# Optimization experiments

Hardware: AMD Instinct MI355X
Metric: run time of the kernel (lower is better)

## Reference

```python
import jax, jax.numpy as jnp
import numpy as np

B, T, D_MODEL = 4, 2048, 1024
D_EXPERT, N_EXPERTS, TOP_K = 4096, 8, 2
CAPACITY_FACTOR = 1.25
AUX_COEFF, Z_COEFF = 0.01, 0.001


def setup_inputs() -> dict:
    key = jax.random.key(0)
    k = jax.random.split(key, 4)
    x = jax.random.normal(k[0], (B, T, D_MODEL), jnp.float32)
    Wr = jax.random.normal(k[1], (D_MODEL, N_EXPERTS), jnp.float32) * 0.02
    W1 = jax.random.normal(k[2], (N_EXPERTS, D_MODEL, D_EXPERT), jnp.float32) * (1.0 / np.sqrt(D_MODEL))
    b1 = jnp.zeros((N_EXPERTS, D_EXPERT), jnp.float32)
    W2 = jax.random.normal(k[3], (N_EXPERTS, D_EXPERT, D_MODEL), jnp.float32) * (1.0 / np.sqrt(D_EXPERT))
    b2 = jnp.zeros((N_EXPERTS, D_MODEL), jnp.float32)
    return {"x": x, "Wr": Wr, "W1": W1, "b1": b1, "W2": W2, "b2": b2}


def reference(x, Wr, W1, b1, W2, b2):
    Bb, Tt, D = x.shape
    N = Bb * Tt
    E = W1.shape[0]
    capacity = max(1, int(N / E * CAPACITY_FACTOR * TOP_K))

    xf = x.reshape(N, D)
    logits = xf @ Wr                                    # (N, E)
    z_loss = jnp.mean(jax.nn.logsumexp(logits, axis=-1) ** 2)
    probs = jax.nn.softmax(logits, axis=-1)             # (N, E)

    topk_p, topk_i = jax.lax.top_k(probs, TOP_K)        # (N, K)
    # one-hot expert mask (top-k experts are distinct per token)
    mask = jnp.zeros((N, E), probs.dtype).at[jnp.arange(N)[:, None], topk_i].set(1.0)

    # capacity truncation: keep first `capacity` assigned tokens per expert, in token order
    pos = (jnp.cumsum(mask, axis=0) - mask).astype(jnp.int32)   # exclusive rank within expert
    keep = (pos < capacity) & (mask > 0)
    mask_t = jnp.where(keep, mask, jnp.zeros_like(mask))

    # Switch-style aux loss on truncated mask
    total_sel = jnp.maximum(mask_t.sum(), 1.0)
    f_i = mask_t.sum(axis=0) / total_sel
    P_i = probs.mean(axis=0)
    aux_loss = E * jnp.sum(f_i * P_i)

    # normalized top-k combine weights (differentiable through probs)
    tk_raw = jnp.take_along_axis(probs, topk_i, axis=1)          # (N, K)
    tk = tk_raw / jnp.maximum(tk_raw.sum(axis=-1, keepdims=True), 1e-9)

    # dispatch tokens into (E, capacity, D) buffer; dropped tokens scatter out of range
    pos_safe = jnp.where(keep, pos, capacity)                    # capacity -> dropped
    pos_k = jnp.take_along_axis(pos_safe, topk_i, axis=1)        # (N, K)
    upd = jnp.broadcast_to(xf[:, None, :], (N, TOP_K, D)).reshape(-1, D)
    buf = jnp.zeros((E, capacity, D), x.dtype).at[topk_i.reshape(-1), pos_k.reshape(-1)].set(upd, mode='drop')

    # grouped expert MLP
    h = jax.nn.relu(jnp.einsum('ecd,edf->ecf', buf, W1) + b1[:, None, :])
    eo = jnp.einsum('ecf,efd->ecd', h, W2) + b2[:, None, :]      # (E, capacity, D)

    # combine: gather each token's top-k expert outputs, weight, sum; dropped -> weight 0
    valid_k = jnp.take_along_axis(keep, topk_i, axis=1)          # (N, K) bool
    w = tk * valid_k.astype(tk.dtype)
    pos_g = jnp.minimum(pos_k, capacity - 1)
    gathered = eo[topk_i, pos_g]                                 # (N, K, D)
    out = jnp.einsum('nk,nkd->nd', w, gathered).reshape(Bb, Tt, D)

    total_aux = AUX_COEFF * aux_loss + Z_COEFF * z_loss
    return out, aux_loss, z_loss, total_aux
```

## Files before the change

kernel.cpp:

```cpp
#include <hip/hip_runtime.h>
#include <stdint.h>

#define N_TOK    8192
#define DM       1024
#define DE       4096
#define NEXP     8
#define CAP      2560
#define AUX_CO   0.01f
#define Z_CO     0.001f

typedef __attribute__((ext_vector_type(4))) float f32x4;
typedef __attribute__((ext_vector_type(8))) __bf16 bf16x8;

static __device__ __forceinline__ unsigned short f2bf(float f) {
  union { float f; uint32_t u; } v; v.f = f;
  uint32_t r = 0x7fffu + ((v.u >> 16) & 1u);
  return (unsigned short)((v.u + r) >> 16);
}
static __device__ __forceinline__ float bf2f(unsigned short u) {
  union { uint32_t u; float f; } v; v.u = ((uint32_t)u) << 16;
  return v.f;
}

#define MEMFENCE() asm volatile("" ::: "memory")
#define BAR()    do { MEMFENCE(); __builtin_amdgcn_s_barrier(); MEMFENCE(); } while (0)
#define LGKM0()  asm volatile("s_waitcnt lgkmcnt(0)" ::: "memory")
#define LGKM8()  asm volatile("s_waitcnt lgkmcnt(8)" ::: "memory")
#define VMW(N)   asm volatile("s_waitcnt vmcnt(" #N ")" ::: "memory")
#define SB0()    __builtin_amdgcn_sched_barrier(0)
#define GLD16(g, l) __builtin_amdgcn_global_load_lds( \
    (const __attribute__((address_space(1))) void*)(g), \
    (__attribute__((address_space(3))) void*)(l), 16, 0, 0)

__global__ __launch_bounds__(256) void transpose_to_bf16(
    const float* __restrict__ in, unsigned short* __restrict__ out, int R, int C)
{
  __shared__ float tile[64][65];
  const size_t eoff = (size_t)blockIdx.z * R * C;
  const int bx = blockIdx.x * 64, by = blockIdx.y * 64;
  const int r = threadIdx.x >> 2, c16 = (threadIdx.x & 3) * 16;
#pragma unroll
  for (int j = 0; j < 4; ++j) {
    const float4 v = *(const float4*)&in[eoff + (size_t)(by + r) * C + bx + c16 + j * 4];
    tile[r][c16 + j * 4 + 0] = v.x; tile[r][c16 + j * 4 + 1] = v.y;
    tile[r][c16 + j * 4 + 2] = v.z; tile[r][c16 + j * 4 + 3] = v.w;
  }
  __syncthreads();
  const int oc = threadIdx.x >> 2, r16 = (threadIdx.x & 3) * 16;
#pragma unroll
  for (int half = 0; half < 2; ++half) {
    uint4 o;
    const int rb = r16 + half * 8;
    o.x = (uint32_t)f2bf(tile[rb + 0][oc]) | ((uint32_t)f2bf(tile[rb + 1][oc]) << 16);
    o.y = (uint32_t)f2bf(tile[rb + 2][oc]) | ((uint32_t)f2bf(tile[rb + 3][oc]) << 16);
    o.z = (uint32_t)f2bf(tile[rb + 4][oc]) | ((uint32_t)f2bf(tile[rb + 5][oc]) << 16);
    o.w = (uint32_t)f2bf(tile[rb + 6][oc]) | ((uint32_t)f2bf(tile[rb + 7][oc]) << 16);
    *(uint4*)&out[eoff + (size_t)(bx + oc) * R + by + rb] = o;
  }
}

__global__ __launch_bounds__(256) void router_kernel(
    const float* __restrict__ x, const float* __restrict__ Wr,
    int* __restrict__ topk, float* __restrict__ tkw, float* __restrict__ zP)
{
  const int tid = threadIdx.x, lane = tid & 63, wave = tid >> 6;
  float zacc = 0.f;
  float pacc[NEXP];
#pragma unroll
  for (int e = 0; e < NEXP; ++e) pacc[e] = 0.f;

  for (int it = 0; it < 4; ++it) {
    const int t = blockIdx.x * 16 + it * 4 + wave;
    float acc[NEXP];
#pragma unroll
    for (int e = 0; e < NEXP; ++e) acc[e] = 0.f;
    const f32x4* x4 = (const f32x4*)(x + (size_t)t * DM);
#pragma unroll
    for (int i = 0; i < 4; ++i) {
      f32x4 xv = x4[i * 64 + lane];
#pragma unroll
      for (int j = 0; j < 4; ++j) {
        const float xs = xv[j];
        const float* wr = Wr + (size_t)((i * 64 + lane) * 4 + j) * NEXP;
#pragma unroll
        for (int e = 0; e < NEXP; ++e) acc[e] += xs * wr[e];
      }
    }
#pragma unroll
    for (int m = 32; m; m >>= 1)
#pragma unroll
      for (int e = 0; e < NEXP; ++e) acc[e] += __shfl_xor(acc[e], m);

    float mx = acc[0];
#pragma unroll
    for (int e = 1; e < NEXP; ++e) mx = fmaxf(mx, acc[e]);
    float p[NEXP], s = 0.f;
#pragma unroll
    for (int e = 0; e < NEXP; ++e) { p[e] = expf(acc[e] - mx); s += p[e]; }
    const float lse = mx + logf(s);
    zacc += lse * lse;
    const float inv_s = 1.f / s;
#pragma unroll
    for (int e = 0; e < NEXP; ++e) pacc[e] += p[e] * inv_s;

    int e0 = 0; float v0 = p[0];
#pragma unroll
    for (int e = 1; e < NEXP; ++e) if (p[e] > v0) { v0 = p[e]; e0 = e; }
    int e1 = -1; float v1 = -1.f;
#pragma unroll
    for (int e = 0; e < NEXP; ++e) if (e != e0 && p[e] > v1) { v1 = p[e]; e1 = e; }

    const float pr0 = v0 * inv_s, pr1 = v1 * inv_s;
    const float denom = fmaxf(pr0 + pr1, 1e-9f);
    if (lane == 0) {
      topk[2*t]   = e0; topk[2*t+1] = e1;
      tkw[2*t]    = pr0 / denom; tkw[2*t+1] = pr1 / denom;
    }
  }
  __shared__ float blk[4][9];
  if (lane == 0) {
    blk[wave][0] = zacc;
#pragma unroll
    for (int e = 0; e < NEXP; ++e) blk[wave][1 + e] = pacc[e];
  }
  __syncthreads();
  if (tid < 9)
    zP[blockIdx.x * 9 + tid] = blk[0][tid] + blk[1][tid] + blk[2][tid] + blk[3][tid];
}

__global__ __launch_bounds__(512) void scan_kernel(
    const int2* __restrict__ topk, const float2* __restrict__ tkw,
    int* __restrict__ posk, float* __restrict__ wts,
    int* __restrict__ inv, int* __restrict__ kept)
{
  __shared__ int2   stopk[N_TOK];
  __shared__ float2 stkw[N_TOK];
  const int tid = threadIdx.x;
  for (int j = tid; j < N_TOK; j += 512) { stopk[j] = topk[j]; stkw[j] = tkw[j]; }
  __syncthreads();

  const int lane = tid & 63;
  const int e = tid >> 6;
  int base = 0;
  const uint64_t below = (lane == 63) ? 0xFFFFFFFFFFFFFFFFull >> 1
                                      : ((1ull << lane) - 1ull);
  for (int i = 0; i < N_TOK / 64; ++i) {
    const int t = i * 64 + lane;
    const int2 ti = stopk[t];
    const float2 w = stkw[t];
    const bool hit = (ti.x == e) || (ti.y == e);
    const uint64_t m = __ballot(hit);
    if (hit) {
      const int pos = base + (int)__popcll(m & below);
      const bool kp = pos < CAP;
      const int k = (ti.x == e) ? 0 : 1;
      posk[2*t + k] = kp ? pos : CAP;
      wts[2*t + k]  = kp ? ((k == 0) ? w.x : w.y) : 0.f;
      if (kp) inv[e * CAP + pos] = t;
    }
    base += (int)__popcll(m);
  }
  const int tail = base < CAP ? base : CAP;
  for (int q = tail + lane; q < CAP; q += 64) inv[e * CAP + q] = -1;
  if (lane == 0) kept[e] = tail;
}

__global__ __launch_bounds__(256) void dispatch_kernel(
    const float* __restrict__ x, const int* __restrict__ inv,
    unsigned short* __restrict__ buf)
{
  const int slot = blockIdx.x;
  const int t = inv[slot];
  ushort4 o;
  if (t >= 0) {
    const f32x4 v = ((const f32x4*)(x + (size_t)t * DM))[threadIdx.x];
    o.x = f2bf(v[0]); o.y = f2bf(v[1]); o.z = f2bf(v[2]); o.w = f2bf(v[3]);
  } else {
    o.x = 0; o.y = 0; o.z = 0; o.w = 0;
  }
  ((ushort4*)(buf + (size_t)slot * DM))[threadIdx.x] = o;
}

template<bool RELU, bool BIAS>
__global__ __launch_bounds__(512, 2) void gemm8p(
    const unsigned short* __restrict__ A,
    const unsigned short* __restrict__ Bt,
    const float* __restrict__ bias,
    unsigned short* __restrict__ C,
    const int* __restrict__ kept,
    int M, int N, int K, int lda, int mt, int nt, int nsplit, int nwg)
{
  __shared__ __attribute__((aligned(16))) unsigned short As[2 * 16384];
  __shared__ __attribute__((aligned(16))) unsigned short Bs[2 * 16384];
  const int tid = threadIdx.x, lane = tid & 63, wave = tid >> 6;
  const int wr = wave >> 2, wc = wave & 3;
  const int frow = lane & 15, kgrp = lane >> 4;

  int wg = (int)blockIdx.x;
  wg = (wg & 7) * (nwg >> 3) + (wg >> 3);
  const int ntpe = mt * nt;
  const int bpe = ntpe * nsplit;
  const int e = wg / bpe;
  const int rem = wg % bpe;
  const int split = rem / ntpe;
  const int rr = rem % ntpe;
  const int m0 = (rr / nt) * 256;
  const int n0 = (rr % nt) * 256;
  if (m0 >= kept[e]) return;

  const unsigned short* Ae = A  + (size_t)e * M * lda + (size_t)m0 * lda + (size_t)split * K;
  const unsigned short* Be = Bt + (size_t)e * N * lda + (size_t)n0 * lda + (size_t)split * K;

  const int srow = tid >> 3;
  const int scol = ((tid & 7) ^ (srow & 7)) * 8;

  auto stA = [&](int t, int h) {
    const int c = t & 1, k0 = t * 64;
#pragma unroll
    for (int i = 0; i < 2; ++i)
      GLD16(Ae + (size_t)(h * 128 + i * 64 + srow) * lda + (k0 + scol),
            &As[c * 16384 + (h * 128 + i * 64) * 64 + tid * 8]);
  };
  auto stB = [&](int t, int h) {
    const int c = t & 1, k0 = t * 64;
#pragma unroll
    for (int i = 0; i < 2; ++i)
      GLD16(Be + (size_t)(h * 128 + i * 64 + srow) * lda + (k0 + scol),
            &Bs[c * 16384 + (h * 128 + i * 64) * 64 + tid * 8]);
  };
  auto rdA = [&](bf16x8* dst, int c, int mh) {
#pragma unroll
    for (int m = 0; m < 4; ++m) {
      const int row = wr * 128 + mh * 64 + m * 16 + frow;
#pragma unroll
      for (int kk = 0; kk < 2; ++kk)
        dst[m * 2 + kk] = *(const bf16x8*)
          &As[c * 16384 + row * 64 + (((kk * 4 + kgrp) ^ (row & 7)) * 8)];
    }
  };
  auto rdB = [&](bf16x8* dst, int c, int nh) {
#pragma unroll
    for (int n = 0; n < 2; ++n) {
      const int row = wc * 64 + nh * 32 + n * 16 + frow;
#pragma unroll
      for (int kk = 0; kk < 2; ++kk)
        dst[n * 2 + kk] = *(const bf16x8*)
          &Bs[c * 16384 + row * 64 + (((kk * 4 + kgrp) ^ (row & 7)) * 8)];
    }
  };

  f32x4 acc[8][4];
#pragma unroll
  for (int m = 0; m < 8; ++m)
#pragma unroll
    for (int n = 0; n < 4; ++n) acc[m][n] = (f32x4){0.f, 0.f, 0.f, 0.f};

  bf16x8 af0[8], af1[8], bq0[4], bq1[4];
  auto mfmaQ = [&](int mh, int nh, bf16x8* af, bf16x8* bq) {
#pragma unroll
    for (int m = 0; m < 4; ++m)
#pragma unroll
      for (int n = 0; n < 2; ++n)
#pragma unroll
        for (int kk = 0; kk < 2; ++kk)
          acc[mh * 4 + m][nh * 2 + n] = __builtin_amdgcn_mfma_f32_16x16x32_bf16(
              af[m * 2 + kk], bq[n * 2 + kk], acc[mh * 4 + m][nh * 2 + n], 0, 0, 0);
  };

  const int nk = K >> 6;

  stA(0, 0); stA(0, 1); stB(0, 0); stB(0, 1);
  stA(1, 0); stA(1, 1); stB(1, 0);
  VMW(6);
  BAR();

  for (int t = 0; t < nk; ++t) {
    const int c = t & 1;
    rdA(af0, c, 0);
    rdB(bq0, c, 0);
    if (t + 1 < nk) stB(t + 1, 1);
    LGKM8();
    BAR(); LGKM0(); SB0();
    __builtin_amdgcn_s_setprio(1);
    mfmaQ(0, 0, af0, bq0);
    __builtin_amdgcn_s_setprio(0);
    BAR();
    rdA(af1, c, 1);
    BAR(); LGKM0(); SB0();
    __builtin_amdgcn_s_setprio(1);
    mfmaQ(1, 0, af1, bq0);
    __builtin_amdgcn_s_setprio(0);
    BAR();
    rdB(bq1, c, 1);
    if (t + 2 < nk) stA(t + 2, 0);
    BAR(); LGKM0(); SB0();
    __builtin_amdgcn_s_setprio(1);
    mfmaQ(0, 1, af0, bq1);
    __builtin_amdgcn_s_setprio(0);
    BAR();
    if (t + 2 < nk) { stA(t + 2, 1); stB(t + 2, 0); }
    BAR(); SB0();
    __builtin_amdgcn_s_setprio(1);
    mfmaQ(1, 1, af1, bq1);
    __builtin_amdgcn_s_setprio(0);
    if (t + 2 < nk)      { VMW(6); }
    else if (t + 1 < nk) { VMW(0); }
    if (t + 1 < nk) BAR();
  }

  unsigned short* Ce = C + (size_t)(split * NEXP + e) * M * N;
  const int r0 = m0 + wr * 128 + 4 * kgrp;
  const int c0 = n0 + wc * 64 + frow;
#pragma unroll
  for (int nf = 0; nf < 4; ++nf) {
    const int cc = c0 + nf * 16;
    float bv = 0.f;
    if (BIAS) bv = bias[(size_t)e * N + cc];
#pragma unroll
    for (int m = 0; m < 8; ++m) {
#pragma unroll
      for (int r = 0; r < 4; ++r) {
        float v = acc[m][nf][r] + bv;
        if (RELU) v = fmaxf(v, 0.f);
        Ce[(size_t)(r0 + m * 16 + r) * N + cc] = f2bf(v);
      }
    }
  }
}

__global__ __launch_bounds__(256) void combine_kernel(
    const unsigned short* __restrict__ eo2,
    const float* __restrict__ b2,
    const int* __restrict__ posk, const float* __restrict__ wts,
    const int* __restrict__ topk,
    const float* __restrict__ zP, const int* __restrict__ kept,
    float* __restrict__ out, float* __restrict__ outs)
{
  const int t = blockIdx.x;
  const int e0 = topk[2*t], e1 = topk[2*t+1];
  int p0 = posk[2*t], p1 = posk[2*t+1];
  p0 = p0 < CAP - 1 ? p0 : CAP - 1;
  p1 = p1 < CAP - 1 ? p1 : CAP - 1;
  const float w0 = wts[2*t], w1 = wts[2*t+1];
  const size_t o0 = ((size_t)e0 * CAP + p0) * DM;
  const size_t o1 = ((size_t)e1 * CAP + p1) * DM;
  const size_t sp = (size_t)NEXP * CAP * DM;
  const ushort4 a0 = ((const ushort4*)(eo2 + o0))[threadIdx.x];
  const ushort4 a1 = ((const ushort4*)(eo2 + sp + o0))[threadIdx.x];
  const ushort4 c0 = ((const ushort4*)(eo2 + o1))[threadIdx.x];
  const ushort4 c1 = ((const ushort4*)(eo2 + sp + o1))[threadIdx.x];
  const f32x4 bv0 = ((const f32x4*)(b2 + (size_t)e0 * DM))[threadIdx.x];
  const f32x4 bv1 = ((const f32x4*)(b2 + (size_t)e1 * DM))[threadIdx.x];
  f32x4 o;
  o[0] = w0 * (bf2f(a0.x) + bf2f(a1.x) + bv0[0]) + w1 * (bf2f(c0.x) + bf2f(c1.x) + bv1[0]);
  o[1] = w0 * (bf2f(a0.y) + bf2f(a1.y) + bv0[1]) + w1 * (bf2f(c0.y) + bf2f(c1.y) + bv1[1]);
  o[2] = w0 * (bf2f(a0.z) + bf2f(a1.z) + bv0[2]) + w1 * (bf2f(c0.z) + bf2f(c1.z) + bv1[2]);
  o[3] = w0 * (bf2f(a0.w) + bf2f(a1.w) + bv0[3]) + w1 * (bf2f(c0.w) + bf2f(c1.w) + bv1[3]);
  ((f32x4*)(out + (size_t)t * DM))[threadIdx.x] = o;

  if (t == 0 && threadIdx.x < 64) {
    const int lane = threadIdx.x;
    float v[9];
#pragma unroll
    for (int e = 0; e < 9; ++e) {
      float s = 0.f;
      for (int bk = 0; bk < 8; ++bk) s += zP[(lane * 8 + bk) * 9 + e];
      v[e] = s;
    }
#pragma unroll
    for (int m = 32; m; m >>= 1)
#pragma unroll
      for (int e = 0; e < 9; ++e) v[e] += __shfl_xor(v[e], m);
    if (lane == 0) {
      const float z = v[0] / (float)N_TOK;
      float total = 0.f;
      for (int e = 0; e < NEXP; ++e) total += (float)kept[e];
      total = fmaxf(total, 1.f);
      float aux = 0.f;
      for (int e = 0; e < NEXP; ++e)
        aux += ((float)kept[e] / total) * (v[1 + e] / (float)N_TOK);
      aux *= (float)NEXP;
      outs[0] = aux;
      outs[1] = z;
      outs[2] = AUX_CO * aux + Z_CO * z;
    }
  }
}

extern "C" void kernel_launch(void* const* d_in, const int* in_sizes, int n_in,
                              void* d_out, int out_size, void* d_ws, size_t ws_size,
                              hipStream_t stream)
{
  const float* x  = (const float*)d_in[0];
  const float* Wr = (const float*)d_in[1];
  const float* W1 = (const float*)d_in[2];
  const float* b1 = (const float*)d_in[3];
  const float* W2 = (const float*)d_in[4];
  const float* b2 = (const float*)d_in[5];
  float* out = (float*)d_out;

  char* p = (char*)d_ws;
  auto alloc = [&](size_t bytes) {
    char* q = p; p += (bytes + 255) & ~(size_t)255; return q;
  };
  unsigned short* W1t = (unsigned short*)alloc((size_t)NEXP * DM * DE * 2);
  unsigned short* W2t = (unsigned short*)alloc((size_t)NEXP * DM * DE * 2);
  unsigned short* buf = (unsigned short*)alloc((size_t)NEXP * CAP * DM * 2);
  unsigned short* h   = (unsigned short*)alloc((size_t)NEXP * CAP * DE * 2);
  unsigned short* eo2 = (unsigned short*)alloc((size_t)2 * NEXP * CAP * DM * 2);
  int*   topk = (int*)alloc((size_t)N_TOK * 2 * 4);
  float* tkw  = (float*)alloc((size_t)N_TOK * 2 * 4);
  int*   posk = (int*)alloc((size_t)N_TOK * 2 * 4);
  float* wts  = (float*)alloc((size_t)N_TOK * 2 * 4);
  int*   inv  = (int*)alloc((size_t)NEXP * CAP * 4);
  int*   kept = (int*)alloc((size_t)NEXP * 4);
  float* zP   = (float*)alloc((size_t)512 * 9 * 4);

  transpose_to_bf16<<<dim3(DE / 64, DM / 64, NEXP), 256, 0, stream>>>(W1, W1t, DM, DE);
  transpose_to_bf16<<<dim3(DM / 64, DE / 64, NEXP), 256, 0, stream>>>(W2, W2t, DE, DM);
  router_kernel<<<512, 256, 0, stream>>>(x, Wr, topk, tkw, zP);
  scan_kernel<<<1, 512, 0, stream>>>((const int2*)topk, (const float2*)tkw, posk, wts, inv, kept);
  dispatch_kernel<<<NEXP * CAP, 256, 0, stream>>>(x, inv, buf);

  gemm8p<true, true><<<1280, 512, 0, stream>>>(
      buf, W1t, b1, h, kept, CAP, DE, DM, DM, 10, 16, 1, 1280);
  gemm8p<false, false><<<640, 512, 0, stream>>>(
      h, W2t, nullptr, eo2, kept, CAP, DM, DE / 2, DE, 10, 4, 2, 640);

  combine_kernel<<<N_TOK, 256, 0, stream>>>(eo2, b2, posk, wts, topk, zP, kept,
                                            out, out + (size_t)N_TOK * DM);
}
```

Measured before the change: 587.7 us.

## Simplify GEMM main loop to two-barrier double-buffered schedule

Swaps the eight-phase ping-pong schedule in the grouped expert GEMM, which interleaved partial LDS loads, partial global stages and MFMA quadrants across many barriers, for a plain double-buffered loop. Each iteration now waits for its tile, reads all A/B fragments from LDS, issues the full next-next stage, then runs all four MFMA quadrants. The aim is fewer barriers and less scheduling overhead per K-step. In exchange it loses the fine-grained overlap of LDS reads with MFMA and holds all fragments live at once, which raises register pressure.

```diff
diff --git a/kernel.cpp b/kernel.cpp
--- a/kernel.cpp
+++ b/kernel.cpp
@@ -25,9 +25,7 @@
 #define MEMFENCE() asm volatile("" ::: "memory")
 #define BAR()    do { MEMFENCE(); __builtin_amdgcn_s_barrier(); MEMFENCE(); } while (0)
 #define LGKM0()  asm volatile("s_waitcnt lgkmcnt(0)" ::: "memory")
-#define LGKM8()  asm volatile("s_waitcnt lgkmcnt(8)" ::: "memory")
 #define VMW(N)   asm volatile("s_waitcnt vmcnt(" #N ")" ::: "memory")
-#define SB0()    __builtin_amdgcn_sched_barrier(0)
 #define GLD16(g, l) __builtin_amdgcn_global_load_lds( \
     (const __attribute__((address_space(1))) void*)(g), \
     (__attribute__((address_space(3))) void*)(l), 16, 0, 0)
@@ -182,7 +180,7 @@
 }
 
 template<bool RELU, bool BIAS>
-__global__ __launch_bounds__(512, 2) void gemm8p(
+__global__ __launch_bounds__(512, 2) void gemm2b(
     const unsigned short* __restrict__ A,
     const unsigned short* __restrict__ Bt,
     const float* __restrict__ bias,
@@ -214,19 +212,16 @@
   const int srow = tid >> 3;
   const int scol = ((tid & 7) ^ (srow & 7)) * 8;
 
-  auto stA = [&](int t, int h) {
+  auto stage = [&](int t) {
     const int c = t & 1, k0 = t * 64;
 #pragma unroll
-    for (int i = 0; i < 2; ++i)
-      GLD16(Ae + (size_t)(h * 128 + i * 64 + srow) * lda + (k0 + scol),
-            &As[c * 16384 + (h * 128 + i * 64) * 64 + tid * 8]);
-  };
-  auto stB = [&](int t, int h) {
-    const int c = t & 1, k0 = t * 64;
-#pragma unroll
-    for (int i = 0; i < 2; ++i)
-      GLD16(Be + (size_t)(h * 128 + i * 64 + srow) * lda + (k0 + scol),
-            &Bs[c * 16384 + (h * 128 + i * 64) * 64 + tid * 8]);
+    for (int i = 0; i < 4; ++i)
+      GLD16(Ae + (size_t)(i * 64 + srow) * lda + (k0 + scol),
+            &As[c * 16384 + i * 4096 + tid * 8]);
+#pragma unroll
+    for (int i = 0; i < 4; ++i)
+      GLD16(Be + (size_t)(i * 64 + srow) * lda + (k0 + scol),
+            &Bs[c * 16384 + i * 4096 + tid * 8]);
   };
   auto rdA = [&](bf16x8* dst, int c, int mh) {
 #pragma unroll
@@ -269,43 +264,25 @@
 
   const int nk = K >> 6;
 
-  stA(0, 0); stA(0, 1); stB(0, 0); stB(0, 1);
-  stA(1, 0); stA(1, 1); stB(1, 0);
-  VMW(6);
-  BAR();
+  stage(0); stage(1);
 
   for (int t = 0; t < nk; ++t) {
     const int c = t & 1;
+    if (t + 2 <= nk) { VMW(8); } else { VMW(0); }
+    BAR();
     rdA(af0, c, 0);
+    rdA(af1, c, 1);
     rdB(bq0, c, 0);
-    if (t + 1 < nk) stB(t + 1, 1);
-    LGKM8();
-    BAR(); LGKM0(); SB0();
+    rdB(bq1, c, 1);
+    LGKM0();
+    BAR();
+    if (t + 2 < nk) stage(t + 2);
     __builtin_amdgcn_s_setprio(1);
     mfmaQ(0, 0, af0, bq0);
-    __builtin_amdgcn_s_setprio(0);
-    BAR();
-    rdA(af1, c, 1);
-    BAR(); LGKM0(); SB0();
-    __builtin_amdgcn_s_setprio(1);
+    mfmaQ(0, 1, af0, bq1);
     mfmaQ(1, 0, af1, bq0);
-    __builtin_amdgcn_s_setprio(0);
-    BAR();
-    rdB(bq1, c, 1);
-    if (t + 2 < nk) stA(t + 2, 0);
-    BAR(); LGKM0(); SB0();
-    __builtin_amdgcn_s_setprio(1);
-    mfmaQ(0, 1, af0, bq1);
-    __builtin_amdgcn_s_setprio(0);
-    BAR();
-    if (t + 2 < nk) { stA(t + 2, 1); stB(t + 2, 0); }
-    BAR(); SB0();
-    __builtin_amdgcn_s_setprio(1);
     mfmaQ(1, 1, af1, bq1);
     __builtin_amdgcn_s_setprio(0);
-    if (t + 2 < nk)      { VMW(6); }
-    else if (t + 1 < nk) { VMW(0); }
-    if (t + 1 < nk) BAR();
   }
 
   unsigned short* Ce = C + (size_t)(split * NEXP + e) * M * N;
@@ -422,9 +399,9 @@
   scan_kernel<<<1, 512, 0, stream>>>((const int2*)topk, (const float2*)tkw, posk, wts, inv, kept);
   dispatch_kernel<<<NEXP * CAP, 256, 0, stream>>>(x, inv, buf);
 
-  gemm8p<true, true><<<1280, 512, 0, stream>>>(
+  gemm2b<true, true><<<1280, 512, 0, stream>>>(
       buf, W1t, b1, h, kept, CAP, DE, DM, DM, 10, 16, 1, 1280);
-  gemm8p<false, false><<<640, 512, 0, stream>>>(
+  gemm2b<false, false><<<640, 512, 0, stream>>>(
       h, W2t, nullptr, eo2, kept, CAP, DM, DE / 2, DE, 10, 4, 2, 640);
 
   combine_kernel<<<N_TOK, 256, 0, stream>>>(eo2, b2, posk, wts, topk, zP, kept,
```

Result: faster. 556.3 us (-5.3%).
